# Performance work log

Measured on AMD Instinct MI355X. Metric: run time of the kernel, lower is better.

Reference implementation:

```python
import jax, jax.numpy as jnp
import numpy as np
from jax import lax

C = 128
HEADS = 8
WS = 8
HIDDEN = C * 4


def _ln2d(x, w, b, eps=1e-6):
    # channel-first LayerNorm over dim 1 of [B,C,H,W]
    u = x.mean(axis=1, keepdims=True)
    s = ((x - u) ** 2).mean(axis=1, keepdims=True)
    xh = (x - u) / jnp.sqrt(s + eps)
    return w[None, :, None, None] * xh + b[None, :, None, None]


def _partition(x, ws):
    # [B,C,H,W] -> [B*nW, ws*ws, C]
    B, C_, H, W = x.shape
    x = x.transpose(0, 2, 3, 1)  # BHWC
    x = x.reshape(B, H // ws, ws, W // ws, ws, C_)
    x = x.transpose(0, 1, 3, 2, 4, 5)
    return x.reshape(-1, ws * ws, C_)


def _reverse(x, ws, H, W, B):
    # [B*nW, ws*ws, C] -> [B,C,H,W]
    C_ = x.shape[-1]
    x = x.reshape(B, H // ws, W // ws, ws, ws, C_)
    x = x.transpose(0, 1, 3, 2, 4, 5).reshape(B, H, W, C_)
    return x.transpose(0, 3, 1, 2)


def setup_inputs() -> dict:
    key = jax.random.key(0)
    ks = jax.random.split(key, 16)
    B, H, W = 4, 256, 256
    inp = {
        "x": jax.random.normal(ks[0], (B, C, H, W), jnp.float32),
        "l0": jax.random.uniform(ks[1], (B, 1, H, W), jnp.float32),
        "norm1_w": jnp.ones((C,), jnp.float32),
        "norm1_b": jnp.zeros((C,), jnp.float32),
        "norm2_w": jnp.ones((C,), jnp.float32),
        "norm2_b": jnp.zeros((C,), jnp.float32),
        "qkv_w": jax.random.normal(ks[2], (3 * C, C), jnp.float32) * (1.0 / np.sqrt(C)),
        "gate_w": jax.random.normal(ks[3], (C,), jnp.float32),
        "gate_b": jnp.zeros((C,), jnp.float32),
        "proj_w": jax.random.normal(ks[4], (C, C), jnp.float32) * (1.0 / np.sqrt(C)),
        "proj_b": jnp.zeros((C,), jnp.float32),
        "ffn_w1": jax.random.normal(ks[5], (HIDDEN, C), jnp.float32) * (1.0 / np.sqrt(C)),
        "ffn_b1": jnp.zeros((HIDDEN,), jnp.float32),
        "ffn_dw": jax.random.normal(ks[6], (HIDDEN, 1, 3, 3), jnp.float32) * (1.0 / 3.0),
        "ffn_dwb": jnp.zeros((HIDDEN,), jnp.float32),
        "ffn_w2": jax.random.normal(ks[7], (C, HIDDEN), jnp.float32) * (1.0 / np.sqrt(HIDDEN)),
        "ffn_b2": jnp.zeros((C,), jnp.float32),
    }
    return inp


def reference(x, l0, norm1_w, norm1_b, norm2_w, norm2_b, qkv_w, gate_w, gate_b,
              proj_w, proj_b, ffn_w1, ffn_b1, ffn_dw, ffn_dwb, ffn_w2, ffn_b2):
    B, C_, H, W = x.shape
    ws = WS
    # H,W chosen divisible by ws -> no padding branch
    head_dim = C_ // HEADS
    scale = head_dim ** -0.5

    shortcut = x
    xn = _ln2d(x, norm1_w, norm1_b)
    qkv = jnp.einsum("oc,bchw->bohw", qkv_w, xn)
    q, k, v = jnp.split(qkv, 3, axis=1)

    # illumination gate (l0 already at [H,W]; bilinear resize to same size is identity)
    gate = jax.nn.sigmoid(l0 * gate_w[None, :, None, None] + gate_b[None, :, None, None])
    q = q * gate

    q = _partition(q, ws)  # [Bw, ws*ws, C]
    k = _partition(k, ws)
    v = _partition(v, ws)
    Bw, N, _ = q.shape
    q = q.reshape(Bw, N, HEADS, head_dim)
    k = k.reshape(Bw, N, HEADS, head_dim)
    v = v.reshape(Bw, N, HEADS, head_dim)

    attn = jnp.einsum("bqhd,bkhd->bhqk", q, k) * scale
    attn = jax.nn.softmax(attn, axis=-1)
    out = jnp.einsum("bhqk,bkhd->bqhd", attn, v).reshape(Bw, N, C_)
    out = _reverse(out, ws, H, W, B)

    out = jnp.einsum("oc,bchw->bohw", proj_w, out) + proj_b[None, :, None, None]
    out = out + shortcut

    # FFN: 1x1 -> GELU -> depthwise 3x3 -> GELU -> 1x1
    h = _ln2d(out, norm2_w, norm2_b)
    h = jnp.einsum("oc,bchw->bohw", ffn_w1, h) + ffn_b1[None, :, None, None]
    h = jax.nn.gelu(h, approximate=False)
    h = lax.conv_general_dilated(h, ffn_dw, window_strides=(1, 1), padding="SAME",
                                 dimension_numbers=("NCHW", "OIHW", "NCHW"),
                                 feature_group_count=HIDDEN)
    h = h + ffn_dwb[None, :, None, None]
    h = jax.nn.gelu(h, approximate=False)
    h = jnp.einsum("oc,bchw->bohw", ffn_w2, h) + ffn_b2[None, :, None, None]
    return out + h
```

## Files before the change

kernel.cpp:

```cpp
#include <hip/hip_runtime.h>
#include <hip/hip_bf16.h>

#define HW   65536
#define CHW  (128*65536)

typedef __attribute__((ext_vector_type(8))) short bf16x8;
typedef __attribute__((ext_vector_type(4))) float f32x4;

__device__ __forceinline__ float geluf(float v){
    float u = 0.7978845608028654f * v * (1.f + 0.044715f*v*v);
    float e = __expf(2.f*u);
    float th = 1.f - 2.f/(e+1.f);
    return 0.5f*v*(1.f+th);
}

__device__ __forceinline__ float sigmoidf_(float z){
    return 1.f / (1.f + __expf(-z));
}

__global__ __launch_bounds__(256) void k_cvt(
    const float* __restrict__ src, __hip_bfloat16* __restrict__ dst, int n)
{
    int i = blockIdx.x*256 + threadIdx.x;
    if (i < n) dst[i] = __float2bfloat16(src[i]);
}

__global__ __launch_bounds__(256,2) void k_ln_qkv_mfma(
    const float* __restrict__ x, const float* __restrict__ l0,
    const float* __restrict__ n1w, const float* __restrict__ n1b,
    const __hip_bfloat16* __restrict__ qkvw, const float* __restrict__ gate_w,
    const float* __restrict__ gate_b, __hip_bfloat16* __restrict__ qkvb)
{
    __shared__ short sxb[128*130];
    __shared__ float sp1[256], sp2[256];
    const int t = threadIdx.x;
    const int lane = t & 63, w = t >> 6;
    const int l15 = lane & 15, q4 = (lane >> 4)*4, ko = (lane >> 4)*8;
    const int mhalf = w & 1, phalf = w >> 1;
    const int pbase = blockIdx.x * 128;
    const int b = pbase >> 16;
    const int hw0 = pbase & 65535;
    const int pxs = t & 127, chalf = t >> 7;
    const float* xb = x + (size_t)b*CHW + (size_t)chalf*64*HW + hw0 + pxs;
    unsigned* srow = (unsigned*)sxb + pxs*65 + chalf*32;

    float s1 = 0.f, s2 = 0.f;
    #pragma unroll 8
    for (int j = 0; j < 32; ++j) {
        float v0 = xb[(size_t)(2*j)*HW];
        float v1 = xb[(size_t)(2*j+1)*HW];
        s1 += v0 + v1; s2 += v0*v0 + v1*v1;
        __hip_bfloat162 pk = __float22bfloat162_rn(make_float2(v0, v1));
        srow[j] = *(unsigned*)&pk;
    }
    sp1[pxs*2 + chalf] = s1;
    sp2[pxs*2 + chalf] = s2;
    __syncthreads();
    const float s1t = sp1[pxs*2] + sp1[pxs*2 + 1];
    const float s2t = sp2[pxs*2] + sp2[pxs*2 + 1];
    const float mean = s1t * 0.0078125f;
    const float rstd = rsqrtf(s2t*0.0078125f - mean*mean + 1e-6f);
    #pragma unroll 8
    for (int j = 0; j < 32; ++j) {
        unsigned u = srow[j];
        float v0 = __uint_as_float(u << 16);
        float v1 = __uint_as_float(u & 0xffff0000u);
        const int c = chalf*64 + 2*j;
        v0 = (v0 - mean)*rstd*n1w[c]   + n1b[c];
        v1 = (v1 - mean)*rstd*n1w[c+1] + n1b[c+1];
        __hip_bfloat162 pk = __float22bfloat162_rn(make_float2(v0, v1));
        srow[j] = *(unsigned*)&pk;
    }
    __syncthreads();

    float lv[4];
    #pragma unroll
    for (int nt = 0; nt < 4; ++nt)
        lv[nt] = l0[(size_t)b*HW + hw0 + phalf*64 + nt*16 + l15];

    const short* wq = (const short*)qkvw;
    for (int oz = 0; oz < 3; ++oz) {
        f32x4 acc[4][4];
        #pragma unroll
        for (int mt = 0; mt < 4; ++mt)
            #pragma unroll
            for (int nt = 0; nt < 4; ++nt)
                acc[mt][nt] = (f32x4){0.f,0.f,0.f,0.f};
        #pragma unroll
        for (int kc = 0; kc < 4; ++kc) {
            bf16x8 bfrag[4];
            #pragma unroll
            for (int nt = 0; nt < 4; ++nt) {
                const int px = phalf*64 + nt*16 + l15;
                bfrag[nt] = *(const bf16x8*)(sxb + px*130 + kc*32 + ko);
            }
            #pragma unroll
            for (int mt = 0; mt < 4; ++mt) {
                const int m = oz*128 + mhalf*64 + mt*16 + l15;
                bf16x8 af = *(const bf16x8*)(wq + m*128 + kc*32 + ko);
                #pragma unroll
                for (int nt = 0; nt < 4; ++nt)
                    acc[mt][nt] = __builtin_amdgcn_mfma_f32_16x16x32_bf16(af, bfrag[nt], acc[mt][nt], 0, 0, 0);
            }
        }
        __hip_bfloat16* ob = qkvb + ((size_t)b*384 + oz*128)*HW + hw0;
        if (oz == 0) {
            #pragma unroll
            for (int mt = 0; mt < 4; ++mt)
                #pragma unroll
                for (int nt = 0; nt < 4; ++nt) {
                    const int px = phalf*64 + nt*16 + l15;
                    #pragma unroll
                    for (int r = 0; r < 4; ++r) {
                        const int o = mhalf*64 + mt*16 + q4 + r;
                        const float g = sigmoidf_(lv[nt]*gate_w[o] + gate_b[o]);
                        ob[(size_t)o*HW + px] = __float2bfloat16(acc[mt][nt][r]*g);
                    }
                }
        } else {
            #pragma unroll
            for (int mt = 0; mt < 4; ++mt)
                #pragma unroll
                for (int nt = 0; nt < 4; ++nt) {
                    const int px = phalf*64 + nt*16 + l15;
                    #pragma unroll
                    for (int r = 0; r < 4; ++r) {
                        const int o = mhalf*64 + mt*16 + q4 + r;
                        ob[(size_t)o*HW + px] = __float2bfloat16(acc[mt][nt][r]);
                    }
                }
        }
    }
}

__global__ __launch_bounds__(64) void k_attn(
    const __hip_bfloat16* __restrict__ qkv, float* __restrict__ attn_out)
{
    __shared__ float sk[64*17];
    __shared__ float sv[64*17];
    const int t = threadIdx.x;
    const int win = blockIdx.x;
    const int head = blockIdx.y;
    const int b = win >> 10;
    const int wi = win & 1023;
    const int wy = wi >> 5, wx = wi & 31;
    const int ty = t >> 3, tx = t & 7;
    const int y = wy*8 + ty, xx = wx*8 + tx;
    const size_t hw = (size_t)y*256 + xx;
    const __hip_bfloat16* qb = qkv + (size_t)b*384*HW + (size_t)head*16*HW + hw;
    const __hip_bfloat16* kb = qb + (size_t)128*HW;
    const __hip_bfloat16* vb = qb + (size_t)256*HW;
    float qr[16];
    #pragma unroll
    for (int d = 0; d < 16; ++d) {
        qr[d]       = __bfloat162float(qb[(size_t)d*HW]);
        sk[t*17+d]  = __bfloat162float(kb[(size_t)d*HW]);
        sv[t*17+d]  = __bfloat162float(vb[(size_t)d*HW]);
    }
    __syncthreads();
    float sc[64];
    float m = -1e30f;
    #pragma unroll
    for (int kt = 0; kt < 64; ++kt) {
        float dot = 0.f;
        #pragma unroll
        for (int d = 0; d < 16; ++d) dot = fmaf(qr[d], sk[kt*17+d], dot);
        dot *= 0.25f;
        sc[kt] = dot;
        m = fmaxf(m, dot);
    }
    float ssum = 0.f;
    #pragma unroll
    for (int kt = 0; kt < 64; ++kt) { float e = __expf(sc[kt]-m); sc[kt] = e; ssum += e; }
    const float rs = 1.f / ssum;
    float o[16];
    #pragma unroll
    for (int d = 0; d < 16; ++d) o[d] = 0.f;
    #pragma unroll
    for (int kt = 0; kt < 64; ++kt) {
        const float p = sc[kt];
        #pragma unroll
        for (int d = 0; d < 16; ++d) o[d] = fmaf(p, sv[kt*17+d], o[d]);
    }
    float* ob = attn_out + (size_t)b*CHW + (size_t)head*16*HW + hw;
    #pragma unroll
    for (int d = 0; d < 16; ++d) ob[(size_t)d*HW] = o[d]*rs;
}

__global__ __launch_bounds__(256,2) void k_proj_mfma(
    const float* __restrict__ x, const __hip_bfloat16* __restrict__ projw,
    const float* __restrict__ proj_b, float* __restrict__ out)
{
    __shared__ short sxb[128*130];
    const int t = threadIdx.x;
    const int lane = t & 63, w = t >> 6;
    const int l15 = lane & 15, q4 = (lane >> 4)*4, ko = (lane >> 4)*8;
    const int mhalf = w & 1, phalf = w >> 1;
    const int pbase = blockIdx.x * 128;
    const int b = pbase >> 16;
    const int hw0 = pbase & 65535;
    const int pxs = t & 127, chalf = t >> 7;
    const float* ab = out + (size_t)b*CHW + (size_t)chalf*64*HW + hw0 + pxs;
    unsigned* srow = (unsigned*)sxb + pxs*65 + chalf*32;
    #pragma unroll 8
    for (int j = 0; j < 32; ++j) {
        float v0 = ab[(size_t)(2*j)*HW];
        float v1 = ab[(size_t)(2*j+1)*HW];
        __hip_bfloat162 pk = __float22bfloat162_rn(make_float2(v0, v1));
        srow[j] = *(unsigned*)&pk;
    }
    __syncthreads();
    f32x4 acc[4][4];
    #pragma unroll
    for (int mt = 0; mt < 4; ++mt)
        #pragma unroll
        for (int nt = 0; nt < 4; ++nt)
            acc[mt][nt] = (f32x4){0.f,0.f,0.f,0.f};
    const short* wp = (const short*)projw;
    #pragma unroll
    for (int kc = 0; kc < 4; ++kc) {
        bf16x8 bfrag[4];
        #pragma unroll
        for (int nt = 0; nt < 4; ++nt) {
            const int px = phalf*64 + nt*16 + l15;
            bfrag[nt] = *(const bf16x8*)(sxb + px*130 + kc*32 + ko);
        }
        #pragma unroll
        for (int mt = 0; mt < 4; ++mt) {
            const int m = mhalf*64 + mt*16 + l15;
            bf16x8 af = *(const bf16x8*)(wp + m*128 + kc*32 + ko);
            #pragma unroll
            for (int nt = 0; nt < 4; ++nt)
                acc[mt][nt] = __builtin_amdgcn_mfma_f32_16x16x32_bf16(af, bfrag[nt], acc[mt][nt], 0, 0, 0);
        }
    }
    const float* xb = x + (size_t)b*CHW + hw0;
    float* ob = out + (size_t)b*CHW + hw0;
    #pragma unroll
    for (int mt = 0; mt < 4; ++mt)
        #pragma unroll
        for (int nt = 0; nt < 4; ++nt) {
            const int px = phalf*64 + nt*16 + l15;
            #pragma unroll
            for (int r = 0; r < 4; ++r) {
                const int o = mhalf*64 + mt*16 + q4 + r;
                ob[(size_t)o*HW + px] = acc[mt][nt][r] + proj_b[o] + xb[(size_t)o*HW + px];
            }
        }
}

__global__ __launch_bounds__(256,2) void k_ffn1_mfma(
    const float* __restrict__ outb, const float* __restrict__ n2w, const float* __restrict__ n2b,
    const __hip_bfloat16* __restrict__ w1, const float* __restrict__ b1,
    __hip_bfloat16* __restrict__ h1s)
{
    __shared__ short sxb[128*130];
    __shared__ float sp1[256], sp2[256];
    const int t = threadIdx.x;
    const int lane = t & 63, w = t >> 6;
    const int l15 = lane & 15, q4 = (lane >> 4)*4, ko = (lane >> 4)*8;
    const int mhalf = w & 1, phalf = w >> 1;
    const int hw0 = blockIdx.x * 128;
    const int pxs = t & 127, chalf = t >> 7;
    const float* xb = outb + (size_t)chalf*64*HW + hw0 + pxs;
    unsigned* srow = (unsigned*)sxb + pxs*65 + chalf*32;
    float s1 = 0.f, s2 = 0.f;
    #pragma unroll 8
    for (int j = 0; j < 32; ++j) {
        float v0 = xb[(size_t)(2*j)*HW];
        float v1 = xb[(size_t)(2*j+1)*HW];
        s1 += v0 + v1; s2 += v0*v0 + v1*v1;
        __hip_bfloat162 pk = __float22bfloat162_rn(make_float2(v0, v1));
        srow[j] = *(unsigned*)&pk;
    }
    sp1[pxs*2 + chalf] = s1;
    sp2[pxs*2 + chalf] = s2;
    __syncthreads();
    const float s1t = sp1[pxs*2] + sp1[pxs*2 + 1];
    const float s2t = sp2[pxs*2] + sp2[pxs*2 + 1];
    const float mean = s1t * 0.0078125f;
    const float rstd = rsqrtf(s2t*0.0078125f - mean*mean + 1e-6f);
    #pragma unroll 8
    for (int j = 0; j < 32; ++j) {
        unsigned u = srow[j];
        float v0 = __uint_as_float(u << 16);
        float v1 = __uint_as_float(u & 0xffff0000u);
        const int c = chalf*64 + 2*j;
        v0 = (v0 - mean)*rstd*n2w[c]   + n2b[c];
        v1 = (v1 - mean)*rstd*n2w[c+1] + n2b[c+1];
        __hip_bfloat162 pk = __float22bfloat162_rn(make_float2(v0, v1));
        srow[j] = *(unsigned*)&pk;
    }
    __syncthreads();
    const short* w1s = (const short*)w1;
    __hip_bfloat16* hb = h1s + hw0;
    for (int mc = 0; mc < 4; ++mc) {
        f32x4 acc[4][4];
        #pragma unroll
        for (int mt = 0; mt < 4; ++mt)
            #pragma unroll
            for (int nt = 0; nt < 4; ++nt)
                acc[mt][nt] = (f32x4){0.f,0.f,0.f,0.f};
        #pragma unroll
        for (int kc = 0; kc < 4; ++kc) {
            bf16x8 bfrag[4];
            #pragma unroll
            for (int nt = 0; nt < 4; ++nt) {
                const int px = phalf*64 + nt*16 + l15;
                bfrag[nt] = *(const bf16x8*)(sxb + px*130 + kc*32 + ko);
            }
            #pragma unroll
            for (int mt = 0; mt < 4; ++mt) {
                const int m = mc*128 + mhalf*64 + mt*16 + l15;
                bf16x8 af = *(const bf16x8*)(w1s + m*128 + kc*32 + ko);
                #pragma unroll
                for (int nt = 0; nt < 4; ++nt)
                    acc[mt][nt] = __builtin_amdgcn_mfma_f32_16x16x32_bf16(af, bfrag[nt], acc[mt][nt], 0, 0, 0);
            }
        }
        #pragma unroll
        for (int mt = 0; mt < 4; ++mt)
            #pragma unroll
            for (int nt = 0; nt < 4; ++nt) {
                const int px = phalf*64 + nt*16 + l15;
                #pragma unroll
                for (int r = 0; r < 4; ++r) {
                    const int o = mc*128 + mhalf*64 + mt*16 + q4 + r;
                    const float v = geluf(acc[mt][nt][r] + b1[o]);
                    hb[(size_t)o*HW + px] = __float2bfloat16(v);
                }
            }
    }
}

__global__ __launch_bounds__(256) void k_dwconv(
    const __hip_bfloat16* __restrict__ h1b,
    unsigned* __restrict__ h2u,
    const float* __restrict__ dwf, const float* __restrict__ dwb)
{
    __shared__ short sh[2*18*260];
    const int t = threadIdx.x;
    const int rb = blockIdx.x & 15;
    const int cp = blockIdx.x >> 4;
    const int row0 = rb * 16;
    #pragma unroll
    for (int ch = 0; ch < 2; ++ch) {
        const __hip_bfloat16* src = h1b + (size_t)(cp*2 + ch)*HW;
        #pragma unroll
        for (int i = 0; i < 9; ++i) {
            const int idx = t + i*256;
            const int r = idx >> 7;
            const int u = idx & 127;
            const int y = row0 - 1 + r;
            unsigned v = 0u;
            if ((unsigned)y < 256u) v = *(const unsigned*)(src + (size_t)y*256 + u*2);
            *(unsigned*)(&sh[ch*4680 + r*260 + 2 + u*2]) = v;
        }
    }
    if (t < 72) {
        const int ch = t / 36, q = t - ch*36;
        const int r = q >> 1;
        sh[ch*4680 + r*260 + ((q & 1) ? 258 : 1)] = 0;
    }
    __syncthreads();
    float wt[2][9], bs[2];
    #pragma unroll
    for (int ch = 0; ch < 2; ++ch) {
        const float* dwc = dwf + (size_t)(cp*2 + ch)*9;
        #pragma unroll
        for (int k = 0; k < 9; ++k) wt[ch][k] = dwc[k];
        bs[ch] = dwb[cp*2 + ch];
    }
    const int xp = (t & 127) * 2;
    const int rh = t >> 7;
    #pragma unroll
    for (int r = 0; r < 8; ++r) {
        const int orow = rh*8 + r;
        const int y = row0 + orow;
        float res[2][2];
        #pragma unroll
        for (int ch = 0; ch < 2; ++ch) {
            const short* base = sh + ch*4680 + orow*260 + xp + 1;
            float a[3][4];
            #pragma unroll
            for (int dy = 0; dy < 3; ++dy)
                #pragma unroll
                for (int k = 0; k < 4; ++k)
                    a[dy][k] = __uint_as_float((unsigned)(unsigned short)base[dy*260 + k] << 16);
            #pragma unroll
            for (int xj = 0; xj < 2; ++xj) {
                float s = bs[ch];
                #pragma unroll
                for (int dy = 0; dy < 3; ++dy)
                    #pragma unroll
                    for (int dx = 0; dx < 3; ++dx)
                        s = fmaf(a[dy][xj+dx], wt[ch][dy*3+dx], s);
                res[ch][xj] = geluf(s);
            }
        }
        __hip_bfloat162 pk0 = __float22bfloat162_rn(make_float2(res[0][0], res[1][0]));
        __hip_bfloat162 pk1 = __float22bfloat162_rn(make_float2(res[0][1], res[1][1]));
        uint2 st;
        st.x = *(unsigned*)&pk0;
        st.y = *(unsigned*)&pk1;
        *(uint2*)(h2u + (size_t)cp*HW + (size_t)y*256 + xp) = st;
    }
}

__global__ __launch_bounds__(256,2) void k_ffn2g(
    const unsigned* __restrict__ h2u, const __hip_bfloat16* __restrict__ w2b,
    const float* __restrict__ b2, float* __restrict__ outb)
{
    __shared__ short sxb[128*130];
    const int t = threadIdx.x;
    const int lane = t & 63, w = t >> 6;
    const int l15 = lane & 15, q4 = (lane >> 4)*4, ko = (lane >> 4)*8;
    const int mhalf = w & 1, phalf = w >> 1;
    const int pbase = blockIdx.x * 128;
    const int pxs = t & 127;
    const int chalf = t >> 7;
    f32x4 acc[4][4];
    #pragma unroll
    for (int mt = 0; mt < 4; ++mt)
        #pragma unroll
        for (int nt = 0; nt < 4; ++nt)
            acc[mt][nt] = (f32x4){0.f,0.f,0.f,0.f};
    const short* w2s = (const short*)w2b;
    for (int k4 = 0; k4 < 4; ++k4) {
        if (k4) __syncthreads();
        const unsigned* hsrc = h2u + (size_t)(k4*64 + chalf*32)*HW + pbase + pxs;
        unsigned* sdst = (unsigned*)sxb + pxs*65 + chalf*32;
        #pragma unroll
        for (int c = 0; c < 32; ++c)
            sdst[c] = hsrc[(size_t)c*HW];
        __syncthreads();
        #pragma unroll
        for (int kc = 0; kc < 4; ++kc) {
            bf16x8 bfrag[4];
            #pragma unroll
            for (int nt = 0; nt < 4; ++nt) {
                const int px = phalf*64 + nt*16 + l15;
                bfrag[nt] = *(const bf16x8*)(sxb + px*130 + kc*32 + ko);
            }
            #pragma unroll
            for (int mt = 0; mt < 4; ++mt) {
                const int m = mhalf*64 + mt*16 + l15;
                bf16x8 af = *(const bf16x8*)(w2s + (size_t)m*512 + k4*128 + kc*32 + ko);
                #pragma unroll
                for (int nt = 0; nt < 4; ++nt)
                    acc[mt][nt] = __builtin_amdgcn_mfma_f32_16x16x32_bf16(af, bfrag[nt], acc[mt][nt], 0, 0, 0);
            }
        }
    }
    #pragma unroll
    for (int mt = 0; mt < 4; ++mt)
        #pragma unroll
        for (int nt = 0; nt < 4; ++nt) {
            const int px = pbase + phalf*64 + nt*16 + l15;
            #pragma unroll
            for (int r = 0; r < 4; ++r) {
                const int o = mhalf*64 + mt*16 + q4 + r;
                outb[(size_t)o*HW + px] = acc[mt][nt][r] + b2[o] + outb[(size_t)o*HW + px];
            }
        }
}

extern "C" void kernel_launch(void* const* d_in, const int* in_sizes, int n_in,
                              void* d_out, int out_size, void* d_ws, size_t ws_size,
                              hipStream_t stream) {
    const float* x      = (const float*)d_in[0];
    const float* l0     = (const float*)d_in[1];
    const float* n1w    = (const float*)d_in[2];
    const float* n1b    = (const float*)d_in[3];
    const float* n2w    = (const float*)d_in[4];
    const float* n2b    = (const float*)d_in[5];
    const float* qkv_w  = (const float*)d_in[6];
    const float* gate_w = (const float*)d_in[7];
    const float* gate_b = (const float*)d_in[8];
    const float* proj_w = (const float*)d_in[9];
    const float* proj_b = (const float*)d_in[10];
    const float* ffn_w1 = (const float*)d_in[11];
    const float* ffn_b1 = (const float*)d_in[12];
    const float* ffn_dw = (const float*)d_in[13];
    const float* ffn_dwb= (const float*)d_in[14];
    const float* ffn_w2 = (const float*)d_in[15];
    const float* ffn_b2 = (const float*)d_in[16];

    float* out = (float*)d_out;
    __hip_bfloat16* qkvb = (__hip_bfloat16*)d_ws;
    unsigned* h2u        = (unsigned*)d_ws;
    __hip_bfloat16* h1s  = (__hip_bfloat16*)((char*)d_ws + 201326592);
    char* wbase = (char*)d_ws + 268435456;
    __hip_bfloat16* qkvw_b = (__hip_bfloat16*)(wbase);
    __hip_bfloat16* projw_b= (__hip_bfloat16*)(wbase + 98304);
    __hip_bfloat16* w1b    = (__hip_bfloat16*)(wbase + 131072);
    __hip_bfloat16* w2b    = (__hip_bfloat16*)(wbase + 262144);

    k_cvt<<<dim3(192), dim3(256), 0, stream>>>(qkv_w, qkvw_b, 49152);
    k_cvt<<<dim3(64),  dim3(256), 0, stream>>>(proj_w, projw_b, 16384);
    k_cvt<<<dim3(256), dim3(256), 0, stream>>>(ffn_w1, w1b, 65536);
    k_cvt<<<dim3(256), dim3(256), 0, stream>>>(ffn_w2, w2b, 65536);

    k_ln_qkv_mfma<<<dim3(2048), dim3(256), 0, stream>>>(x, l0, n1w, n1b, qkvw_b, gate_w, gate_b, qkvb);
    k_attn       <<<dim3(4096, 8), dim3(64), 0, stream>>>(qkvb, out);
    k_proj_mfma  <<<dim3(2048), dim3(256), 0, stream>>>(x, projw_b, proj_b, out);
    for (int b = 0; b < 4; ++b) {
        k_ffn1_mfma<<<dim3(512),  dim3(256), 0, stream>>>(out + (size_t)b*CHW, n2w, n2b, w1b, ffn_b1, h1s);
        k_dwconv   <<<dim3(4096), dim3(256), 0, stream>>>(h1s, h2u, ffn_dw, ffn_dwb);
        k_ffn2g    <<<dim3(512),  dim3(256), 0, stream>>>(h2u, w2b, ffn_b2, out + (size_t)b*CHW);
    }
}
```

Baseline: 1.285 ms.

## Store QKV in window-partitioned head-major layout for vectorized attention loads

Result: faster. 1.230 ms (-4.3%).

```diff
diff --git a/kernel.cpp b/kernel.cpp
--- a/kernel.cpp
+++ b/kernel.cpp
@@ -3,6 +3,9 @@
 
 #define HW   65536
 #define CHW  (128*65536)
+#define QKV_OZ  33554432u
+#define QKV_H   1048576u
+#define QKV_WIN 1024u
 
 typedef __attribute__((ext_vector_type(8))) short bf16x8;
 typedef __attribute__((ext_vector_type(4))) float f32x4;
@@ -16,6 +19,10 @@
 
 __device__ __forceinline__ float sigmoidf_(float z){
     return 1.f / (1.f + __expf(-z));
+}
+
+__device__ __forceinline__ float bf2f(short s){
+    return __uint_as_float(((unsigned)(unsigned short)s) << 16);
 }
 
 __global__ __launch_bounds__(256) void k_cvt(
@@ -40,6 +47,9 @@
     const int pbase = blockIdx.x * 128;
     const int b = pbase >> 16;
     const int hw0 = pbase & 65535;
+    const int x0 = hw0 & 255;
+    const int y  = hw0 >> 8;
+    const int wy = y >> 3, ty = y & 7;
     const int pxs = t & 127, chalf = t >> 7;
     const float* xb = x + (size_t)b*CHW + (size_t)chalf*64*HW + hw0 + pxs;
     unsigned* srow = (unsigned*)sxb + pxs*65 + chalf*32;
@@ -78,6 +88,13 @@
     for (int nt = 0; nt < 4; ++nt)
         lv[nt] = l0[(size_t)b*HW + hw0 + phalf*64 + nt*16 + l15];
 
+    unsigned toff[4];
+    #pragma unroll
+    for (int nt = 0; nt < 4; ++nt) {
+        const int xg = x0 + phalf*64 + nt*16 + l15;
+        toff[nt] = (unsigned)((wy*32 + (xg >> 3))*1024 + (ty*8 + (xg & 7))*16);
+    }
+
     const short* wq = (const short*)qkvw;
     for (int oz = 0; oz < 3; ++oz) {
         f32x4 acc[4][4];
@@ -103,32 +120,28 @@
                     acc[mt][nt] = __builtin_amdgcn_mfma_f32_16x16x32_bf16(af, bfrag[nt], acc[mt][nt], 0, 0, 0);
             }
         }
-        __hip_bfloat16* ob = qkvb + ((size_t)b*384 + oz*128)*HW + hw0;
-        if (oz == 0) {
-            #pragma unroll
-            for (int mt = 0; mt < 4; ++mt)
-                #pragma unroll
-                for (int nt = 0; nt < 4; ++nt) {
-                    const int px = phalf*64 + nt*16 + l15;
-                    #pragma unroll
-                    for (int r = 0; r < 4; ++r) {
-                        const int o = mhalf*64 + mt*16 + q4 + r;
-                        const float g = sigmoidf_(lv[nt]*gate_w[o] + gate_b[o]);
-                        ob[(size_t)o*HW + px] = __float2bfloat16(acc[mt][nt][r]*g);
-                    }
+        __hip_bfloat16* ob = qkvb + (size_t)oz*QKV_OZ + (size_t)b*8*QKV_H;
+        #pragma unroll
+        for (int mt = 0; mt < 4; ++mt) {
+            const int h = mhalf*4 + mt;
+            #pragma unroll
+            for (int nt = 0; nt < 4; ++nt) {
+                float v0 = acc[mt][nt][0], v1 = acc[mt][nt][1];
+                float v2 = acc[mt][nt][2], v3 = acc[mt][nt][3];
+                if (oz == 0) {
+                    const int o = h*16 + q4;
+                    v0 *= sigmoidf_(lv[nt]*gate_w[o]   + gate_b[o]);
+                    v1 *= sigmoidf_(lv[nt]*gate_w[o+1] + gate_b[o+1]);
+                    v2 *= sigmoidf_(lv[nt]*gate_w[o+2] + gate_b[o+2]);
+                    v3 *= sigmoidf_(lv[nt]*gate_w[o+3] + gate_b[o+3]);
                 }
-        } else {
-            #pragma unroll
-            for (int mt = 0; mt < 4; ++mt)
-                #pragma unroll
-                for (int nt = 0; nt < 4; ++nt) {
-                    const int px = phalf*64 + nt*16 + l15;
-                    #pragma unroll
-                    for (int r = 0; r < 4; ++r) {
-                        const int o = mhalf*64 + mt*16 + q4 + r;
-                        ob[(size_t)o*HW + px] = __float2bfloat16(acc[mt][nt][r]);
-                    }
-                }
+                __hip_bfloat162 p0 = __float22bfloat162_rn(make_float2(v0, v1));
+                __hip_bfloat162 p1 = __float22bfloat162_rn(make_float2(v2, v3));
+                uint2 st;
+                st.x = *(unsigned*)&p0;
+                st.y = *(unsigned*)&p1;
+                *(uint2*)(ob + (size_t)h*QKV_H + toff[nt] + q4) = st;
+            }
         }
     }
 }
@@ -143,19 +156,25 @@
     const int head = blockIdx.y;
     const int b = win >> 10;
     const int wi = win & 1023;
-    const int wy = wi >> 5, wx = wi & 31;
-    const int ty = t >> 3, tx = t & 7;
-    const int y = wy*8 + ty, xx = wx*8 + tx;
-    const size_t hw = (size_t)y*256 + xx;
-    const __hip_bfloat16* qb = qkv + (size_t)b*384*HW + (size_t)head*16*HW + hw;
-    const __hip_bfloat16* kb = qb + (size_t)128*HW;
-    const __hip_bfloat16* vb = qb + (size_t)256*HW;
+    const size_t wb = ((size_t)(b*8 + head))*QKV_H + (size_t)wi*QKV_WIN + t*16;
+    const __hip_bfloat16* qp = qkv + wb;
+    const __hip_bfloat16* kp = qp + QKV_OZ;
+    const __hip_bfloat16* vp = qp + 2u*QKV_OZ;
+    bf16x8 q0 = *(const bf16x8*)(qp);
+    bf16x8 q1 = *(const bf16x8*)(qp + 8);
+    bf16x8 k0 = *(const bf16x8*)(kp);
+    bf16x8 k1 = *(const bf16x8*)(kp + 8);
+    bf16x8 v0 = *(const bf16x8*)(vp);
+    bf16x8 v1 = *(const bf16x8*)(vp + 8);
     float qr[16];
     #pragma unroll
-    for (int d = 0; d < 16; ++d) {
-        qr[d]       = __bfloat162float(qb[(size_t)d*HW]);
-        sk[t*17+d]  = __bfloat162float(kb[(size_t)d*HW]);
-        sv[t*17+d]  = __bfloat162float(vb[(size_t)d*HW]);
+    for (int j = 0; j < 8; ++j) {
+        qr[j]   = bf2f(q0[j]);
+        qr[8+j] = bf2f(q1[j]);
+        sk[t*17 + j]     = bf2f(k0[j]);
+        sk[t*17 + 8 + j] = bf2f(k1[j]);
+        sv[t*17 + j]     = bf2f(v0[j]);
+        sv[t*17 + 8 + j] = bf2f(v1[j]);
     }
     __syncthreads();
     float sc[64];
@@ -182,6 +201,9 @@
         #pragma unroll
         for (int d = 0; d < 16; ++d) o[d] = fmaf(p, sv[kt*17+d], o[d]);
     }
+    const int wy = wi >> 5, wx = wi & 31;
+    const int ty = t >> 3, tx = t & 7;
+    const size_t hw = (size_t)(wy*8 + ty)*256 + wx*8 + tx;
     float* ob = attn_out + (size_t)b*CHW + (size_t)head*16*HW + hw;
     #pragma unroll
     for (int d = 0; d < 16; ++d) ob[(size_t)d*HW] = o[d]*rs;
```
